# Kernel tuning notes

Hardware: AMD Instinct MI355X
Metric: run time of the kernel (lower is better)

Reference implementation:

```python
import jax, jax.numpy as jnp
import numpy as np

B, S, D_IN, D_ATT = 8, 2048, 512, 512
D_ROT = D_ATT // 2  # RotaryEmbedding(dim=attention_dim//2): only first half of features rotated


def _rotary(x):
    # x: [B, S, D_ATT]; rotate first D_ROT dims with interleaved-pair rotation (lucidrains style)
    seq = x.shape[1]
    inv_freq = 1.0 / (10000.0 ** (jnp.arange(0, D_ROT, 2, dtype=jnp.float32) / D_ROT))  # [D_ROT/2]
    freqs = jnp.arange(seq, dtype=jnp.float32)[:, None] * inv_freq[None, :]             # [S, D_ROT/2]
    freqs = jnp.repeat(freqs, 2, axis=-1)                                               # [S, D_ROT]
    cos, sin = jnp.cos(freqs), jnp.sin(freqs)
    xr = x[..., :D_ROT]
    x1, x2 = xr[..., 0::2], xr[..., 1::2]
    rot = jnp.stack((-x2, x1), axis=-1).reshape(xr.shape)  # rotate_half, interleaved pairs
    return jnp.concatenate([xr * cos + rot * sin, x[..., D_ROT:]], axis=-1)


def setup_inputs() -> dict:
    key = jax.random.key(0)
    ks = jax.random.split(key, 10)
    s = 1.0 / np.sqrt(D_IN)
    return {
        "query": jax.random.normal(ks[0], (B, S, D_IN), dtype=jnp.float32),
        "key": jax.random.normal(ks[1], (B, S, D_IN), dtype=jnp.float32),
        "value": jax.random.normal(ks[2], (B, S, D_IN), dtype=jnp.float32),
        "mask": jax.random.randint(ks[3], (B, S, S), 0, 2, dtype=jnp.int32),
        "Wq": jax.random.uniform(ks[4], (D_IN, D_ATT), jnp.float32, -s, s),
        "bq": jnp.zeros((D_ATT,), jnp.float32),
        "Wk": jax.random.uniform(ks[5], (D_IN, D_ATT), jnp.float32, -s, s),
        "bk": jnp.zeros((D_ATT,), jnp.float32),
        "Wv": jax.random.uniform(ks[6], (D_IN, D_ATT), jnp.float32, -s, s),
        "bv": jnp.zeros((D_ATT,), jnp.float32),
    }


def reference(query, key, value, mask, Wq, bq, Wk, bk, Wv, bv):
    q = query @ Wq + bq
    k = key @ Wk + bk
    v = value @ Wv + bv
    q = _rotary(q)
    k = _rotary(k)
    scores = jnp.einsum("bqd,bkd->bqk", q, k) / jnp.float32(np.sqrt(D_ATT))
    # faithful to source: masked positions get -1e-9 (note: source likely meant -1e9)
    scores = jnp.where(mask == 0, jnp.float32(-1e-9), scores)
    weights = jax.nn.softmax(scores, axis=-1)
    context = jnp.einsum("bqk,bkd->bqd", weights, v)
    return context, weights
```

## Files before the change

### kernel.cpp

```cpp
#include <hip/hip_runtime.h>
#include <hip/hip_bf16.h>
#include <hip/hip_fp16.h>

#define B_   8
#define S_   2048
#define DIN  512
#define DATT 512
#define DROT 256

typedef __attribute__((ext_vector_type(4))) float f32x4;
typedef __attribute__((ext_vector_type(8))) short bf16x8;
typedef __attribute__((ext_vector_type(8))) unsigned short u16x8;

__device__ __forceinline__ short f2bf(float f) {
    __hip_bfloat16 h = __float2bfloat16(f);
    return *reinterpret_cast<short*>(&h);
}
__device__ __forceinline__ unsigned short f2h(float f) {
    __half h = __float2half(f);
    return *reinterpret_cast<unsigned short*>(&h);
}
__device__ __forceinline__ float h2f(unsigned short u) {
    __half h = *reinterpret_cast<__half*>(&u);
    return __half2float(h);
}

__global__ void k_tables(float* __restrict__ cosT, float* __restrict__ sinT) {
    int idx = blockIdx.x * 256 + threadIdx.x;
    if (idx >= S_ * 128) return;
    int s = idx >> 7;
    int i = idx & 127;
    float e    = (float)(2 * i) / (float)DROT;
    float invf = 1.0f / powf(10000.0f, e);
    float f    = (float)s * invf;
    float c = cosf(f), sn = sinf(f);
    cosT[s * 256 + 2 * i]     = c;
    cosT[s * 256 + 2 * i + 1] = c;
    sinT[s * 256 + 2 * i]     = sn;
    sinT[s * 256 + 2 * i + 1] = sn;
}

__global__ __launch_bounds__(256) void k_wt(
    const float* __restrict__ Wq, const float* __restrict__ Wk,
    const float* __restrict__ Wv,
    short* __restrict__ WtQ, short* __restrict__ WtK, short* __restrict__ WtV)
{
    const float* W; short* Wt;
    if (blockIdx.y == 0)      { W = Wq; Wt = WtQ; }
    else if (blockIdx.y == 1) { W = Wk; Wt = WtK; }
    else                      { W = Wv; Wt = WtV; }
    int kt = blockIdx.x & 7, nt = blockIdx.x >> 3;
    int k0 = kt * 64, n0 = nt * 64;
    __shared__ float tile[64 * 68];
    int t = threadIdx.x;
    #pragma unroll
    for (int i = 0; i < 4; ++i) {
        int slot = t + 256 * i;
        int row = slot >> 4;
        int c4  = (slot & 15) * 4;
        float4 v = *(const float4*)&W[(size_t)(k0 + row) * DATT + n0 + c4];
        *(float4*)&tile[row * 68 + c4] = v;
    }
    __syncthreads();
    int nr = t >> 2, kq = (t & 3) * 16;
    bf16x8 o0, o1;
    #pragma unroll
    for (int j = 0; j < 8; ++j) o0[j] = f2bf(tile[(kq + j) * 68 + nr]);
    #pragma unroll
    for (int j = 0; j < 8; ++j) o1[j] = f2bf(tile[(kq + 8 + j) * 68 + nr]);
    *(bf16x8*)&Wt[(size_t)(n0 + nr) * DIN + k0 + kq]     = o0;
    *(bf16x8*)&Wt[(size_t)(n0 + nr) * DIN + k0 + kq + 8] = o1;
}

__global__ __launch_bounds__(256) void k_proj3(
    const float* __restrict__ Xq, const float* __restrict__ Xk,
    const float* __restrict__ Xv, const short* __restrict__ Wt0,
    const float* __restrict__ bq, const float* __restrict__ bk,
    const float* __restrict__ bv,
    short* __restrict__ Qb, short* __restrict__ Kb, short* __restrict__ Vb,
    const float* __restrict__ cosT, const float* __restrict__ sinT)
{
    int z = blockIdx.z;
    const float* X    = (z == 0) ? Xq : (z == 1) ? Xk : Xv;
    const float* bias = (z == 0) ? bq : (z == 1) ? bk : bv;
    short*       Out  = (z == 0) ? Qb : (z == 1) ? Kb : Vb;
    const short* Wt   = Wt0 + (size_t)z * DATT * DIN;
    int doRot = (z < 2);

    __shared__ __align__(16) float smem[8704];
    short* As = (short*)smem;
    short* Bs = (short*)(smem + 4608);
    float* Ct = smem;
    int t = threadIdx.x;
    int l = t & 63, w = t >> 6;
    int wr = (w >> 1) * 64, wc = (w & 1) * 64;
    int fr = l & 15, fk8 = (l >> 4) * 8;
    int xr = (fr & 7) << 3;
    int rowBase = blockIdx.y * 128;
    int nBase   = blockIdx.x * 128;

    f32x4 acc[4][4] = {};
    int trA = t >> 4, tcA = (t & 15) * 4;
    int srow = w * 8 + (l >> 3);
    int skolsw = (((l & 7) ^ (l >> 3)) * 8);

    for (int k0 = 0; k0 < DIN; k0 += 64) {
        #pragma unroll
        for (int it = 0; it < 4; ++it) {
            int r = it * 32 + srow;
            __builtin_amdgcn_global_load_lds(
                (const __attribute__((address_space(1))) void*)
                    &Wt[(size_t)(nBase + r) * DIN + k0 + skolsw],
                (__attribute__((address_space(3))) void*)
                    &Bs[(it * 32 + w * 8) * 64],
                16, 0, 0);
        }
        #pragma unroll
        for (int ii = 0; ii < 8; ++ii) {
            int r = ii * 16 + trA;
            float4 v = *(const float4*)&X[(size_t)(rowBase + r) * DIN + k0 + tcA];
            short4 s4 = make_short4(f2bf(v.x), f2bf(v.y), f2bf(v.z), f2bf(v.w));
            *(short4*)&As[r * 72 + tcA] = s4;
        }
        __syncthreads();
        #pragma unroll
        for (int kk = 0; kk < 64; kk += 32) {
            bf16x8 af[4], bfr[4];
            #pragma unroll
            for (int m = 0; m < 4; ++m)
                af[m] = *(const bf16x8*)&As[(wr + m * 16 + fr) * 72 + kk + fk8];
            #pragma unroll
            for (int n = 0; n < 4; ++n)
                bfr[n] = *(const bf16x8*)&Bs[(wc + n * 16 + fr) * 64 + ((kk + fk8) ^ xr)];
            #pragma unroll
            for (int m = 0; m < 4; ++m)
                #pragma unroll
                for (int n = 0; n < 4; ++n)
                    acc[m][n] = __builtin_amdgcn_mfma_f32_16x16x32_bf16(af[m], bfr[n], acc[m][n], 0, 0, 0);
        }
        __syncthreads();
    }

    for (int ch = 0; ch < 4; ++ch) {
        if ((w & 1) == (ch >> 1)) {
            int nb = (ch & 1) * 2;
            #pragma unroll
            for (int n2 = 0; n2 < 2; ++n2)
                #pragma unroll
                for (int m = 0; m < 4; ++m)
                    #pragma unroll
                    for (int q = 0; q < 4; ++q)
                        Ct[(wr + m * 16 + (l >> 4) * 4 + q) * 34 + n2 * 16 + fr]
                            = acc[m][nb + n2][q];
        }
        __syncthreads();
        {
            int r = t >> 1, seg = (t & 1) * 16;
            int rg = rowBase + r;
            int cg = nBase + ch * 32 + seg;
            float vv[16];
            #pragma unroll
            for (int u = 0; u < 4; ++u)
                *(float4*)&vv[4 * u] = *(float4*)&Ct[r * 34 + seg + 4 * u];
            #pragma unroll
            for (int u = 0; u < 4; ++u) {
                float4 bb = *(const float4*)&bias[cg + 4 * u];
                vv[4 * u + 0] += bb.x; vv[4 * u + 1] += bb.y;
                vv[4 * u + 2] += bb.z; vv[4 * u + 3] += bb.w;
            }
            if (doRot && cg < DROT) {
                int s = rg & (S_ - 1);
                float cs[16], sn[16];
                #pragma unroll
                for (int u = 0; u < 4; ++u) {
                    *(float4*)&cs[4 * u] = *(const float4*)&cosT[s * 256 + cg + 4 * u];
                    *(float4*)&sn[4 * u] = *(const float4*)&sinT[s * 256 + cg + 4 * u];
                }
                #pragma unroll
                for (int j = 0; j < 16; j += 2) {
                    float x1 = vv[j], x2 = vv[j + 1];
                    vv[j]     = x1 * cs[j]     - x2 * sn[j];
                    vv[j + 1] = x2 * cs[j + 1] + x1 * sn[j + 1];
                }
            }
            bf16x8 o0, o1;
            #pragma unroll
            for (int j = 0; j < 8; ++j) { o0[j] = f2bf(vv[j]); o1[j] = f2bf(vv[8 + j]); }
            *(bf16x8*)&Out[(size_t)rg * DATT + cg]     = o0;
            *(bf16x8*)&Out[(size_t)rg * DATT + cg + 8] = o1;
        }
        __syncthreads();
    }
}

__global__ __launch_bounds__(256) void k_vt(
    const short* __restrict__ Vb, short* __restrict__ Vt)
{
    int b = blockIdx.z;
    int d0 = blockIdx.x * 64;
    int r0 = blockIdx.y * 64;
    const short* Vp = Vb + (size_t)b * S_ * DATT;
    short* Tp = Vt + (size_t)b * DATT * S_;
    __shared__ short tile[64 * 66];
    int t = threadIdx.x;
    #pragma unroll
    for (int i = 0; i < 2; ++i) {
        int slot = t + 256 * i;
        int row = slot >> 3;
        int c8  = (slot & 7) * 8;
        bf16x8 v = *(const bf16x8*)&Vp[(size_t)(r0 + row) * DATT + d0 + c8];
        #pragma unroll
        for (int j = 0; j < 8; ++j) tile[row * 66 + c8 + j] = v[j];
    }
    __syncthreads();
    int dr = t >> 2, rq = (t & 3) * 16;
    bf16x8 o0, o1;
    #pragma unroll
    for (int j = 0; j < 8; ++j) o0[j] = tile[(rq + j) * 66 + dr];
    #pragma unroll
    for (int j = 0; j < 8; ++j) o1[j] = tile[(rq + 8 + j) * 66 + dr];
    *(bf16x8*)&Tp[(size_t)(d0 + dr) * S_ + r0 + rq]     = o0;
    *(bf16x8*)&Tp[(size_t)(d0 + dr) * S_ + r0 + rq + 8] = o1;
}

__global__ __launch_bounds__(256) void k_scores_h(
    const short* __restrict__ Qb, const short* __restrict__ Kb,
    unsigned short* __restrict__ Sraw)
{
    __shared__ __align__(16) float smem[8192];
    short* As = (short*)smem;
    short* Bs = (short*)(smem + 4096);
    float* Ct = smem;
    int t = threadIdx.x;
    int l = t & 63, w = t >> 6;
    int wr = (w >> 1) * 64, wc = (w & 1) * 64;
    int fr = l & 15, fk8 = (l >> 4) * 8;
    int xr = (fr & 7) << 3;
    int b = blockIdx.z;
    int iBase = blockIdx.y * 128;
    int jBase = blockIdx.x * 128;
    const short* Qp = Qb + (size_t)b * S_ * DATT;
    const short* Kp = Kb + (size_t)b * S_ * DATT;

    f32x4 acc[4][4] = {};
    int srow = w * 8 + (l >> 3);
    int skolsw = (((l & 7) ^ (l >> 3)) * 8);

    for (int k0 = 0; k0 < DATT; k0 += 64) {
        #pragma unroll
        for (int it = 0; it < 4; ++it) {
            int r = it * 32 + srow;
            __builtin_amdgcn_global_load_lds(
                (const __attribute__((address_space(1))) void*)
                    &Qp[(size_t)(iBase + r) * DATT + k0 + skolsw],
                (__attribute__((address_space(3))) void*)
                    &As[(it * 32 + w * 8) * 64],
                16, 0, 0);
            __builtin_amdgcn_global_load_lds(
                (const __attribute__((address_space(1))) void*)
                    &Kp[(size_t)(jBase + r) * DATT + k0 + skolsw],
                (__attribute__((address_space(3))) void*)
                    &Bs[(it * 32 + w * 8) * 64],
                16, 0, 0);
        }
        __syncthreads();
        #pragma unroll
        for (int kk = 0; kk < 64; kk += 32) {
            bf16x8 af[4], bfr[4];
            #pragma unroll
            for (int m = 0; m < 4; ++m)
                af[m] = *(const bf16x8*)&As[(wr + m * 16 + fr) * 64 + ((kk + fk8) ^ xr)];
            #pragma unroll
            for (int n = 0; n < 4; ++n)
                bfr[n] = *(const bf16x8*)&Bs[(wc + n * 16 + fr) * 64 + ((kk + fk8) ^ xr)];
            #pragma unroll
            for (int m = 0; m < 4; ++m)
                #pragma unroll
                for (int n = 0; n < 4; ++n)
                    acc[m][n] = __builtin_amdgcn_mfma_f32_16x16x32_bf16(af[m], bfr[n], acc[m][n], 0, 0, 0);
        }
        __syncthreads();
    }

    const float scale = 0.04419417382415922f;
    for (int ch = 0; ch < 4; ++ch) {
        if ((w & 1) == (ch >> 1)) {
            int nb = (ch & 1) * 2;
            #pragma unroll
            for (int n2 = 0; n2 < 2; ++n2)
                #pragma unroll
                for (int m = 0; m < 4; ++m)
                    #pragma unroll
                    for (int q = 0; q < 4; ++q)
                        Ct[(wr + m * 16 + (l >> 4) * 4 + q) * 34 + n2 * 16 + fr]
                            = acc[m][nb + n2][q] * scale;
        }
        __syncthreads();
        {
            int r = t >> 1, seg = (t & 1) * 16;
            size_t base = ((size_t)b * S_ + iBase + r) * S_ + jBase + ch * 32 + seg;
            float vv[16];
            #pragma unroll
            for (int u = 0; u < 4; ++u)
                *(float4*)&vv[4 * u] = *(float4*)&Ct[r * 34 + seg + 4 * u];
            u16x8 h0, h1;
            #pragma unroll
            for (int j = 0; j < 8; ++j) { h0[j] = f2h(vv[j]); h1[j] = f2h(vv[8 + j]); }
            *(u16x8*)&Sraw[base]     = h0;
            *(u16x8*)&Sraw[base + 8] = h1;
        }
        __syncthreads();
    }
}

__global__ __launch_bounds__(256) void k_softmax_h(
    unsigned short* __restrict__ SrawPb, const int* __restrict__ mask,
    float* __restrict__ wts)
{
    size_t row = blockIdx.x;
    unsigned short* sp = SrawPb + row * S_;
    const int* mp = mask + row * S_;
    float* wp = wts + row * S_;
    int t = threadIdx.x, l = t & 63, w = t >> 6;

    u16x8 raw = *(const u16x8*)&sp[8 * t];
    int4 m0 = *(const int4*)&mp[8 * t];
    int4 m1 = *(const int4*)&mp[8 * t + 4];
    float v[8];
    v[0] = (m0.x == 0) ? -1e-9f : h2f(raw[0]);
    v[1] = (m0.y == 0) ? -1e-9f : h2f(raw[1]);
    v[2] = (m0.z == 0) ? -1e-9f : h2f(raw[2]);
    v[3] = (m0.w == 0) ? -1e-9f : h2f(raw[3]);
    v[4] = (m1.x == 0) ? -1e-9f : h2f(raw[4]);
    v[5] = (m1.y == 0) ? -1e-9f : h2f(raw[5]);
    v[6] = (m1.z == 0) ? -1e-9f : h2f(raw[6]);
    v[7] = (m1.w == 0) ? -1e-9f : h2f(raw[7]);

    float mx = v[0];
    #pragma unroll
    for (int j = 1; j < 8; ++j) mx = fmaxf(mx, v[j]);
    for (int off = 32; off; off >>= 1) mx = fmaxf(mx, __shfl_xor(mx, off));
    __shared__ float red[8];
    if (l == 0) red[w] = mx;
    __syncthreads();
    mx = fmaxf(fmaxf(red[0], red[1]), fmaxf(red[2], red[3]));
    float sum = 0.f;
    #pragma unroll
    for (int j = 0; j < 8; ++j) { v[j] = expf(v[j] - mx); sum += v[j]; }
    for (int off = 32; off; off >>= 1) sum += __shfl_xor(sum, off);
    if (l == 0) red[4 + w] = sum;
    __syncthreads();
    sum = red[4] + red[5] + red[6] + red[7];
    float inv = 1.0f / sum;
    #pragma unroll
    for (int j = 0; j < 8; ++j) v[j] *= inv;

    *(float4*)&wp[8 * t]     = make_float4(v[0], v[1], v[2], v[3]);
    *(float4*)&wp[8 * t + 4] = make_float4(v[4], v[5], v[6], v[7]);
    bf16x8 pb8;
    #pragma unroll
    for (int j = 0; j < 8; ++j) pb8[j] = f2bf(v[j]);
    *(bf16x8*)&sp[8 * t] = pb8;
}

__global__ __launch_bounds__(256) void k_ctx_bf16(
    const short* __restrict__ Pb, const short* __restrict__ Vt,
    float* __restrict__ ctx)
{
    __shared__ __align__(16) float smem[8192];
    short* As = (short*)smem;
    short* Bs = (short*)(smem + 4096);
    float* Ct = smem;
    int t = threadIdx.x;
    int l = t & 63, w = t >> 6;
    int wr = (w >> 1) * 64, wc = (w & 1) * 64;
    int fr = l & 15, fk8 = (l >> 4) * 8;
    int xr = (fr & 7) << 3;
    int b = blockIdx.z;
    int iBase = blockIdx.y * 128;
    int nBase = blockIdx.x * 128;
    const short* Ap = Pb + (size_t)b * S_ * S_;
    const short* Bp = Vt + (size_t)b * DATT * S_;

    f32x4 acc[4][4] = {};
    int srow = w * 8 + (l >> 3);
    int skolsw = (((l & 7) ^ (l >> 3)) * 8);

    for (int k0 = 0; k0 < S_; k0 += 64) {
        #pragma unroll
        for (int it = 0; it < 4; ++it) {
            int r = it * 32 + srow;
            __builtin_amdgcn_global_load_lds(
                (const __attribute__((address_space(1))) void*)
                    &Ap[(size_t)(iBase + r) * S_ + k0 + skolsw],
                (__attribute__((address_space(3))) void*)
                    &As[(it * 32 + w * 8) * 64],
                16, 0, 0);
            __builtin_amdgcn_global_load_lds(
                (const __attribute__((address_space(1))) void*)
                    &Bp[(size_t)(nBase + r) * S_ + k0 + skolsw],
                (__attribute__((address_space(3))) void*)
                    &Bs[(it * 32 + w * 8) * 64],
                16, 0, 0);
        }
        __syncthreads();
        #pragma unroll
        for (int kk = 0; kk < 64; kk += 32) {
            bf16x8 af[4], bfr[4];
            #pragma unroll
            for (int m = 0; m < 4; ++m)
                af[m] = *(const bf16x8*)&As[(wr + m * 16 + fr) * 64 + ((kk + fk8) ^ xr)];
            #pragma unroll
            for (int n = 0; n < 4; ++n)
                bfr[n] = *(const bf16x8*)&Bs[(wc + n * 16 + fr) * 64 + ((kk + fk8) ^ xr)];
            #pragma unroll
            for (int m = 0; m < 4; ++m)
                #pragma unroll
                for (int n = 0; n < 4; ++n)
                    acc[m][n] = __builtin_amdgcn_mfma_f32_16x16x32_bf16(af[m], bfr[n], acc[m][n], 0, 0, 0);
        }
        __syncthreads();
    }

    for (int ch = 0; ch < 4; ++ch) {
        if ((w & 1) == (ch >> 1)) {
            int nb = (ch & 1) * 2;
            #pragma unroll
            for (int n2 = 0; n2 < 2; ++n2)
                #pragma unroll
                for (int m = 0; m < 4; ++m)
                    #pragma unroll
                    for (int q = 0; q < 4; ++q)
                        Ct[(wr + m * 16 + (l >> 4) * 4 + q) * 34 + n2 * 16 + fr]
                            = acc[m][nb + n2][q];
        }
        __syncthreads();
        {
            int r = t >> 1, seg = (t & 1) * 16;
            int gi = iBase + r;
            size_t base = ((size_t)b * S_ + gi) * DATT + nBase + ch * 32 + seg;
            #pragma unroll
            for (int u = 0; u < 4; ++u) {
                float4 vv = *(float4*)&Ct[r * 34 + seg + 4 * u];
                *(float4*)&ctx[base + 4 * u] = vv;
            }
        }
        __syncthreads();
    }
}

__global__ __launch_bounds__(256) void k_scores_f32(
    const short* __restrict__ Qb, const short* __restrict__ Kb,
    const int* __restrict__ mask, float* __restrict__ wOut)
{
    __shared__ __align__(16) float smem[4352];
    short* As = (short*)smem;
    short* Bs = (short*)(smem + 2048);
    float* Ct = smem;
    int t = threadIdx.x;
    int l = t & 63, w = t >> 6;
    int wr = (w >> 1) * 64, wc = (w & 1) * 64;
    int fr = l & 15, fk = (l >> 4) * 8;
    int b = blockIdx.z;
    int iBase = blockIdx.y * 128;
    int jBase = blockIdx.x * 128;
    const short* Qp = Qb + (size_t)b * S_ * DATT;
    const short* Kp = Kb + (size_t)b * S_ * DATT;

    f32x4 acc[4][4] = {};
    int srow = w * 16 + (l >> 2);
    int skol = (l & 3) * 8;

    for (int k0 = 0; k0 < DATT; k0 += 32) {
        #pragma unroll
        for (int it = 0; it < 2; ++it) {
            int r = it * 64 + srow;
            __builtin_amdgcn_global_load_lds(
                (const __attribute__((address_space(1))) void*)
                    &Qp[(size_t)(iBase + r) * DATT + k0 + skol],
                (__attribute__((address_space(3))) void*)
                    &As[(it * 64 + w * 16) * 32],
                16, 0, 0);
            __builtin_amdgcn_global_load_lds(
                (const __attribute__((address_space(1))) void*)
                    &Kp[(size_t)(jBase + r) * DATT + k0 + skol],
                (__attribute__((address_space(3))) void*)
                    &Bs[(it * 64 + w * 16) * 32],
                16, 0, 0);
        }
        __syncthreads();
        bf16x8 af[4], bfr[4];
        #pragma unroll
        for (int m = 0; m < 4; ++m)
            af[m] = *(const bf16x8*)&As[(wr + m * 16 + fr) * 32 + fk];
        #pragma unroll
        for (int n = 0; n < 4; ++n)
            bfr[n] = *(const bf16x8*)&Bs[(wc + n * 16 + fr) * 32 + fk];
        #pragma unroll
        for (int m = 0; m < 4; ++m)
            #pragma unroll
            for (int n = 0; n < 4; ++n)
                acc[m][n] = __builtin_amdgcn_mfma_f32_16x16x32_bf16(af[m], bfr[n], acc[m][n], 0, 0, 0);
        __syncthreads();
    }

    const float scale = 0.04419417382415922f;
    for (int ch = 0; ch < 4; ++ch) {
        if ((w & 1) == (ch >> 1)) {
            int nb = (ch & 1) * 2;
            #pragma unroll
            for (int n2 = 0; n2 < 2; ++n2)
                #pragma unroll
                for (int m = 0; m < 4; ++m)
                    #pragma unroll
                    for (int q = 0; q < 4; ++q)
                        Ct[(wr + m * 16 + (l >> 4) * 4 + q) * 34 + n2 * 16 + fr]
                            = acc[m][nb + n2][q] * scale;
        }
        __syncthreads();
        {
            int r = t >> 1, seg = (t & 1) * 16;
            size_t base = ((size_t)b * S_ + iBase + r) * S_ + jBase + ch * 32 + seg;
            #pragma unroll
            for (int u = 0; u < 4; ++u) {
                float4 vv = *(float4*)&Ct[r * 34 + seg + 4 * u];
                int4  mm = *(const int4*)&mask[base + 4 * u];
                vv.x = (mm.x == 0) ? -1e-9f : vv.x;
                vv.y = (mm.y == 0) ? -1e-9f : vv.y;
                vv.z = (mm.z == 0) ? -1e-9f : vv.z;
                vv.w = (mm.w == 0) ? -1e-9f : vv.w;
                *(float4*)&wOut[base + 4 * u] = vv;
            }
        }
        __syncthreads();
    }
}

__global__ __launch_bounds__(256) void k_softmax_f32(float* __restrict__ wts) {
    size_t row = blockIdx.x;
    float* p = wts + row * S_;
    int t = threadIdx.x, l = t & 63, w = t >> 6;
    float v[8];
    *(float4*)&v[0] = ((const float4*)p)[t];
    *(float4*)&v[4] = ((const float4*)p)[t + 256];
    float mx = v[0];
    #pragma unroll
    for (int j = 1; j < 8; ++j) mx = fmaxf(mx, v[j]);
    for (int off = 32; off; off >>= 1) mx = fmaxf(mx, __shfl_xor(mx, off));
    __shared__ float red[8];
    if (l == 0) red[w] = mx;
    __syncthreads();
    mx = fmaxf(fmaxf(red[0], red[1]), fmaxf(red[2], red[3]));
    float sum = 0.f;
    #pragma unroll
    for (int j = 0; j < 8; ++j) { v[j] = expf(v[j] - mx); sum += v[j]; }
    for (int off = 32; off; off >>= 1) sum += __shfl_xor(sum, off);
    if (l == 0) red[4 + w] = sum;
    __syncthreads();
    sum = red[4] + red[5] + red[6] + red[7];
    float inv = 1.0f / sum;
    #pragma unroll
    for (int j = 0; j < 8; ++j) v[j] *= inv;
    ((float4*)p)[t]       = *(float4*)&v[0];
    ((float4*)p)[t + 256] = *(float4*)&v[4];
}

__global__ __launch_bounds__(256) void k_ctx_f32(
    const float* __restrict__ wts, const short* __restrict__ Vt,
    float* __restrict__ ctx)
{
    __shared__ short As[128 * 40];
    __shared__ short Bs[128 * 32];
    int t = threadIdx.x;
    int l = t & 63, w = t >> 6;
    int wr = (w >> 1) * 64, wc = (w & 1) * 64;
    int fr = l & 15, fk = (l >> 4) * 8;
    int b = blockIdx.z;
    int iBase = blockIdx.y * 128;
    int nBase = blockIdx.x * 128;
    const float* Wp = wts + (size_t)b * S_ * S_;
    const short* Bp = Vt + (size_t)b * DATT * S_;

    f32x4 acc[4][4] = {};
    int trA = t >> 3, tcA = (t & 7) * 4;
    int srow = w * 16 + (l >> 2), skol = (l & 3) * 8;

    for (int k0 = 0; k0 < S_; k0 += 32) {
        #pragma unroll
        for (int it = 0; it < 2; ++it) {
            int r = it * 64 + srow;
            __builtin_amdgcn_global_load_lds(
                (const __attribute__((address_space(1))) void*)
                    &Bp[(size_t)(nBase + r) * S_ + k0 + skol],
                (__attribute__((address_space(3))) void*)
                    &Bs[(it * 64 + w * 16) * 32],
                16, 0, 0);
        }
        #pragma unroll
        for (int ii = 0; ii < 4; ++ii) {
            int r = trA + 32 * ii;
            float4 v = *(const float4*)&Wp[(size_t)(iBase + r) * S_ + k0 + tcA];
            short4 s4 = make_short4(f2bf(v.x), f2bf(v.y), f2bf(v.z), f2bf(v.w));
            *(short4*)&As[r * 40 + tcA] = s4;
        }
        __syncthreads();
        bf16x8 af[4], bfr[4];
        #pragma unroll
        for (int m = 0; m < 4; ++m)
            af[m] = *(const bf16x8*)&As[(wr + m * 16 + fr) * 40 + fk];
        #pragma unroll
        for (int n = 0; n < 4; ++n)
            bfr[n] = *(const bf16x8*)&Bs[(wc + n * 16 + fr) * 32 + fk];
        #pragma unroll
        for (int m = 0; m < 4; ++m)
            #pragma unroll
            for (int n = 0; n < 4; ++n)
                acc[m][n] = __builtin_amdgcn_mfma_f32_16x16x32_bf16(af[m], bfr[n], acc[m][n], 0, 0, 0);
        __syncthreads();
    }

    for (int m = 0; m < 4; ++m) {
        for (int q = 0; q < 4; ++q) {
            int i = iBase + wr + m * 16 + (l >> 4) * 4 + q;
            for (int n = 0; n < 4; ++n) {
                int d = nBase + wc + n * 16 + fr;
                ctx[((size_t)b * S_ + i) * DATT + d] = acc[m][n][q];
            }
        }
    }
}

extern "C" void kernel_launch(void* const* d_in, const int* in_sizes, int n_in,
                              void* d_out, int out_size, void* d_ws, size_t ws_size,
                              hipStream_t stream) {
    const float* query = (const float*)d_in[0];
    const float* key   = (const float*)d_in[1];
    const float* value = (const float*)d_in[2];
    const int*   mask  = (const int*)d_in[3];
    const float* Wq = (const float*)d_in[4];
    const float* bq = (const float*)d_in[5];
    const float* Wk = (const float*)d_in[6];
    const float* bk = (const float*)d_in[7];
    const float* Wv = (const float*)d_in[8];
    const float* bv = (const float*)d_in[9];

    float* ctx = (float*)d_out;
    float* wts = ctx + (size_t)B_ * S_ * DATT;

    char* ws = (char*)d_ws;
    const size_t SZ_QKV = (size_t)B_ * S_ * DATT * 2;
    const size_t SZ_WT  = (size_t)DATT * DIN * 2;
    const size_t SZ_TAB = (size_t)S_ * 256 * 4;
    short* Qb   = (short*)(ws);
    short* Kb   = (short*)(ws + SZ_QKV);
    short* Vt   = (short*)(ws + 2 * SZ_QKV);
    short* WtQ  = (short*)(ws + 3 * SZ_QKV);
    float* cosT = (float*)(ws + 3 * SZ_QKV + 3 * SZ_WT);
    float* sinT = (float*)(ws + 3 * SZ_QKV + 3 * SZ_WT + SZ_TAB);
    char*  big  = ws + 3 * SZ_QKV + 3 * SZ_WT + 2 * SZ_TAB;
    short* Vb   = (short*)big;
    unsigned short* Sraw = (unsigned short*)big;
    const size_t needA = 3 * SZ_QKV + 3 * SZ_WT + 2 * SZ_TAB
                       + (size_t)B_ * S_ * S_ * 2;
    int useH = ws_size >= needA ? 1 : 0;

    short* WtK = WtQ + (size_t)DATT * DIN;
    short* WtV = WtK + (size_t)DATT * DIN;

    k_tables<<<dim3((S_ * 128) / 256), 256, 0, stream>>>(cosT, sinT);
    k_wt<<<dim3(64, 3), 256, 0, stream>>>(Wq, Wk, Wv, WtQ, WtK, WtV);
    k_proj3<<<dim3(4, 128, 3), 256, 0, stream>>>(query, key, value, WtQ,
                                                 bq, bk, bv, Qb, Kb, Vb,
                                                 cosT, sinT);
    k_vt<<<dim3(8, 32, 8), 256, 0, stream>>>(Vb, Vt);
    if (useH) {
        k_scores_h<<<dim3(16, 16, 8), 256, 0, stream>>>(Qb, Kb, Sraw);
        k_softmax_h<<<dim3(B_ * S_), 256, 0, stream>>>(Sraw, mask, wts);
        k_ctx_bf16<<<dim3(4, 16, 8), 256, 0, stream>>>((short*)Sraw, Vt, ctx);
    } else {
        k_scores_f32<<<dim3(16, 16, 8), 256, 0, stream>>>(Qb, Kb, mask, wts);
        k_softmax_f32<<<dim3(B_ * S_), 256, 0, stream>>>(wts);
        k_ctx_f32<<<dim3(4, 16, 8), 256, 0, stream>>>(wts, Vt, ctx);
    }
}
```

Before: 524.3 us.

## Remap GEMM block IDs for XCD-aware L2 locality and merge prep kernels

Fuses the rotary table kernel and the weight transpose kernel into a single launch, which saves one kernel launch. It also remaps the flat block index in the projection, scores and context GEMMs so that the blocks sent round-robin to each of the 8 XCDs get contiguous tiles. The aim is for blocks sharing A/B operand rows to land on the same XCD's L2 and raise hit rates. The cost is a little extra index arithmetic, and the benefit depends on the hardware actually dispatching blocks round-robin across XCDs.

```diff
diff --git a/kernel.cpp b/kernel.cpp
--- a/kernel.cpp
+++ b/kernel.cpp
@@ -25,34 +25,38 @@
     return __half2float(h);
 }
 
-__global__ void k_tables(float* __restrict__ cosT, float* __restrict__ sinT) {
-    int idx = blockIdx.x * 256 + threadIdx.x;
-    if (idx >= S_ * 128) return;
-    int s = idx >> 7;
-    int i = idx & 127;
-    float e    = (float)(2 * i) / (float)DROT;
-    float invf = 1.0f / powf(10000.0f, e);
-    float f    = (float)s * invf;
-    float c = cosf(f), sn = sinf(f);
-    cosT[s * 256 + 2 * i]     = c;
-    cosT[s * 256 + 2 * i + 1] = c;
-    sinT[s * 256 + 2 * i]     = sn;
-    sinT[s * 256 + 2 * i + 1] = sn;
-}
-
-__global__ __launch_bounds__(256) void k_wt(
+__global__ __launch_bounds__(256) void k_prep(
+    float* __restrict__ cosT, float* __restrict__ sinT,
     const float* __restrict__ Wq, const float* __restrict__ Wk,
     const float* __restrict__ Wv,
     short* __restrict__ WtQ, short* __restrict__ WtK, short* __restrict__ WtV)
 {
+    __shared__ float tile[64 * 68];
+    int bid = blockIdx.x;
+    int t = threadIdx.x;
+    if (bid < 1024) {
+        int idx = bid * 256 + t;
+        int s = idx >> 7;
+        int i = idx & 127;
+        float e    = (float)(2 * i) / (float)DROT;
+        float invf = 1.0f / powf(10000.0f, e);
+        float f    = (float)s * invf;
+        float c = cosf(f), sn = sinf(f);
+        cosT[s * 256 + 2 * i]     = c;
+        cosT[s * 256 + 2 * i + 1] = c;
+        sinT[s * 256 + 2 * i]     = sn;
+        sinT[s * 256 + 2 * i + 1] = sn;
+        return;
+    }
+    int wi = bid - 1024;
+    int mz = wi >> 6;
+    int xi = wi & 63;
     const float* W; short* Wt;
-    if (blockIdx.y == 0)      { W = Wq; Wt = WtQ; }
-    else if (blockIdx.y == 1) { W = Wk; Wt = WtK; }
-    else                      { W = Wv; Wt = WtV; }
-    int kt = blockIdx.x & 7, nt = blockIdx.x >> 3;
+    if (mz == 0)      { W = Wq; Wt = WtQ; }
+    else if (mz == 1) { W = Wk; Wt = WtK; }
+    else              { W = Wv; Wt = WtV; }
+    int kt = xi & 7, nt = xi >> 3;
     int k0 = kt * 64, n0 = nt * 64;
-    __shared__ float tile[64 * 68];
-    int t = threadIdx.x;
     #pragma unroll
     for (int i = 0; i < 4; ++i) {
         int slot = t + 256 * i;
@@ -80,7 +84,13 @@
     short* __restrict__ Qb, short* __restrict__ Kb, short* __restrict__ Vb,
     const float* __restrict__ cosT, const float* __restrict__ sinT)
 {
-    int z = blockIdx.z;
+    int fid = blockIdx.x + 4 * (blockIdx.y + 128 * blockIdx.z);
+    fid = (fid & 7) * 192 + (fid >> 3);
+    int bx = fid & 3;
+    int rem = fid >> 2;
+    int by = rem & 127;
+    int z  = rem >> 7;
+
     const float* X    = (z == 0) ? Xq : (z == 1) ? Xk : Xv;
     const float* bias = (z == 0) ? bq : (z == 1) ? bk : bv;
     short*       Out  = (z == 0) ? Qb : (z == 1) ? Kb : Vb;
@@ -96,8 +106,8 @@
     int wr = (w >> 1) * 64, wc = (w & 1) * 64;
     int fr = l & 15, fk8 = (l >> 4) * 8;
     int xr = (fr & 7) << 3;
-    int rowBase = blockIdx.y * 128;
-    int nBase   = blockIdx.x * 128;
+    int rowBase = by * 128;
+    int nBase   = bx * 128;
 
     f32x4 acc[4][4] = {};
     int trA = t >> 4, tcA = (t & 15) * 4;
@@ -227,6 +237,13 @@
     const short* __restrict__ Qb, const short* __restrict__ Kb,
     unsigned short* __restrict__ Sraw)
 {
+    int fid = blockIdx.x + 16 * (blockIdx.y + 16 * blockIdx.z);
+    fid = (fid & 7) * 256 + (fid >> 3);
+    int bxs = fid & 15;
+    int rem = fid >> 4;
+    int bys = rem & 15;
+    int b   = rem >> 4;
+
     __shared__ __align__(16) float smem[8192];
     short* As = (short*)smem;
     short* Bs = (short*)(smem + 4096);
@@ -236,9 +253,8 @@
     int wr = (w >> 1) * 64, wc = (w & 1) * 64;
     int fr = l & 15, fk8 = (l >> 4) * 8;
     int xr = (fr & 7) << 3;
-    int b = blockIdx.z;
-    int iBase = blockIdx.y * 128;
-    int jBase = blockIdx.x * 128;
+    int iBase = bys * 128;
+    int jBase = bxs * 128;
     const short* Qp = Qb + (size_t)b * S_ * DATT;
     const short* Kp = Kb + (size_t)b * S_ * DATT;
 
@@ -367,6 +383,13 @@
     const short* __restrict__ Pb, const short* __restrict__ Vt,
     float* __restrict__ ctx)
 {
+    int fid = blockIdx.x + 4 * (blockIdx.y + 16 * blockIdx.z);
+    fid = (fid & 7) * 64 + (fid >> 3);
+    int bxs = fid & 3;
+    int rem = fid >> 2;
+    int bys = rem & 15;
+    int b   = rem >> 4;
+
     __shared__ __align__(16) float smem[8192];
     short* As = (short*)smem;
     short* Bs = (short*)(smem + 4096);
@@ -376,9 +399,8 @@
     int wr = (w >> 1) * 64, wc = (w & 1) * 64;
     int fr = l & 15, fk8 = (l >> 4) * 8;
     int xr = (fr & 7) << 3;
-    int b = blockIdx.z;
-    int iBase = blockIdx.y * 128;
-    int nBase = blockIdx.x * 128;
+    int iBase = bys * 128;
+    int nBase = bxs * 128;
     const short* Ap = Pb + (size_t)b * S_ * S_;
     const short* Bp = Vt + (size_t)b * DATT * S_;
 
@@ -667,8 +689,7 @@
     short* WtK = WtQ + (size_t)DATT * DIN;
     short* WtV = WtK + (size_t)DATT * DIN;
 
-    k_tables<<<dim3((S_ * 128) / 256), 256, 0, stream>>>(cosT, sinT);
-    k_wt<<<dim3(64, 3), 256, 0, stream>>>(Wq, Wk, Wv, WtQ, WtK, WtV);
+    k_prep<<<dim3(1216), 256, 0, stream>>>(cosT, sinT, Wq, Wk, Wv, WtQ, WtK, WtV);
     k_proj3<<<dim3(4, 128, 3), 256, 0, stream>>>(query, key, value, WtQ,
                                                  bq, bk, bv, Qb, Kb, Vb,
                                                  cosT, sinT);
```

Result: no change. 519.7 us (-0.9%).
